# Kernel tuning notes

Hardware: AMD Instinct MI355X
Metric: run time of the kernel (lower is better)

## Reference

```python
import jax, jax.numpy as jnp
import numpy as np

B, H, W, D = 4, 256, 256, 128  # batch, height, width, channels (dim)
PAD = 1  # mask_padding -> band half-width


def setup_inputs() -> dict:
    key = jax.random.key(0)
    ks = jax.random.split(key, 6)
    s = 0.05  # weight init scale
    return {
        "x": jax.random.normal(ks[0], (B, H, W, D), jnp.float32),
        "kv": jax.random.normal(ks[1], (B, H, W, D), jnp.float32),
        "Wq_h": jax.random.normal(ks[2], (D, D), jnp.float32) * s,
        "Wk_h": jax.random.normal(ks[3], (D, D), jnp.float32) * s,
        "Wq_w": jax.random.normal(ks[4], (D, D), jnp.float32) * s,
        "Wk_w": jax.random.normal(ks[5], (D, D), jnp.float32) * s,
    }


def _band_mask(t, pad, dtype):
    # Equivalent to conv2d(identity, horizontal-line kernel): 1 where |i-j| <= pad
    i = jnp.arange(t)
    return (jnp.abs(i[:, None] - i[None, :]) <= pad).astype(dtype)


def _attend(xa, kva, Wq, Wk, pad):
    # xa, kva: [N, t, d]; heads==1 so dim_heads == d (per source early-return quirk)
    q = xa @ Wq.T                                   # [N, t, d]
    k = kva @ Wk.T                                  # [N, t, d]
    e = q.shape[-1]
    dots = jnp.einsum('bie,bje->bij', q, k) * (e ** -0.5)  # [N, t, t]
    mask = _band_mask(dots.shape[-1], pad, dots.dtype)
    dots = dots + (1.0 - mask) * (-30000.0)
    attn = jax.nn.softmax(dots, axis=-1)
    # NOTE: original multiplies attention weights with raw kv (not v projection)
    return jnp.einsum('bij,bjd->bid', attn, kva)    # [N, t, d]


def reference(x, kv, Wq_h, Wk_h, Wq_w, Wk_w):
    b, h, w, d = x.shape
    # Axis 1 (height): permutation [0,2,1,3]
    xh = jnp.transpose(x, (0, 2, 1, 3)).reshape(b * w, h, d)
    kvh = jnp.transpose(kv, (0, 2, 1, 3)).reshape(b * w, h, d)
    oh = _attend(xh, kvh, Wq_h, Wk_h, PAD).reshape(b, w, h, d)
    oh = jnp.transpose(oh, (0, 2, 1, 3))
    # Axis 2 (width): identity permutation [0,1,2,3]
    xw = x.reshape(b * h, w, d)
    kvw = kv.reshape(b * h, w, d)
    ow = _attend(xw, kvw, Wq_w, Wk_w, PAD).reshape(b, h, w, d)
    return oh + ow  # sum_axial_out=True
```

## Files before the change

kernel.cpp:

```cpp
#include <hip/hip_runtime.h>

#define DD    128
#define LINE  256
#define NPOS  262144
#define TILE  64
#define NROW  66
#define NROWP 80
#define LSTR  136

typedef __bf16 bf16x8 __attribute__((ext_vector_type(8)));
typedef float  f32x4v __attribute__((ext_vector_type(4)));
typedef float  f32x2v __attribute__((ext_vector_type(2)));
typedef unsigned int u32x2v __attribute__((ext_vector_type(2)));
typedef unsigned int u32x4v __attribute__((ext_vector_type(4)));

static __device__ __forceinline__ unsigned short f2bf(float f) {
  union { float f; unsigned u; } v; v.f = f;
  unsigned u = v.u + 0x7FFFu + ((v.u >> 16) & 1u);
  return (unsigned short)(u >> 16);
}
#define BF_LO(u) __uint_as_float((u) << 16)
#define BF_HI(u) __uint_as_float((u) & 0xffff0000u)


__global__ void make_mt_kernel(const float* __restrict__ Wq_h, const float* __restrict__ Wk_h,
                               const float* __restrict__ Wq_w, const float* __restrict__ Wk_w,
                               unsigned short* __restrict__ Ms) {
  const float* Wq = blockIdx.y ? Wq_w : Wq_h;
  const float* Wk = blockIdx.y ? Wk_w : Wk_h;
  unsigned short* M = Ms + blockIdx.y * (DD * DD);
  int d = blockIdx.x, c = threadIdx.x;
  float acc = 0.f;
  for (int e = 0; e < DD; ++e) acc += Wq[e * DD + c] * Wk[e * DD + d];
  M[d * DD + c] = f2bf(acc * 0.08838834764831845f);
}

__global__ __launch_bounds__(256) void project_kernel(const float* __restrict__ x,
                                                      const unsigned short* __restrict__ Mt,
                                                      unsigned short* __restrict__ XMh,
                                                      unsigned short* __restrict__ XMw) {
  __shared__ unsigned short x_s[64 * LSTR];
  const int tid = threadIdx.x;
  const long row0 = (long)blockIdx.x * 64;

  for (int u = tid; u < 64 * 32; u += 256) {
    int row = u >> 5, c4 = u & 31;
    f32x4v v = *(const f32x4v*)(x + (row0 + row) * DD + c4 * 4);
    u32x2v wv;
    wv.x = (unsigned)f2bf(v.x) | ((unsigned)f2bf(v.y) << 16);
    wv.y = (unsigned)f2bf(v.z) | ((unsigned)f2bf(v.w) << 16);
    *(u32x2v*)&x_s[row * LSTR + c4 * 4] = wv;
  }
  __syncthreads();

  const int wave = tid >> 6, lane = tid & 63;
  const int r16 = lane & 15, q = lane >> 4;
  const unsigned short* Mm = Mt + (wave >> 1) * (DD * DD);
  unsigned short* XO = (wave >> 1) ? XMw : XMh;

#pragma unroll
  for (int ci = 0; ci < 4; ++ci) {
    int ct = (wave & 1) * 4 + ci;
    bf16x8 b[4];
#pragma unroll
    for (int ks = 0; ks < 4; ++ks)
      b[ks] = __builtin_bit_cast(
          bf16x8, *(const u32x4v*)(Mm + (ct * 16 + r16) * DD + ks * 32 + q * 8));
#pragma unroll
    for (int rt = 0; rt < 4; ++rt) {
      f32x4v acc = {0.f, 0.f, 0.f, 0.f};
#pragma unroll
      for (int ks = 0; ks < 4; ++ks) {
        bf16x8 a = __builtin_bit_cast(
            bf16x8, *(const u32x4v*)&x_s[(rt * 16 + r16) * LSTR + ks * 32 + q * 8]);
        acc = __builtin_amdgcn_mfma_f32_16x16x32_bf16(a, b[ks], acc, 0, 0, 0);
      }
#pragma unroll
      for (int r = 0; r < 4; ++r) {
        long row = row0 + rt * 16 + q * 4 + r;
        XO[row * DD + ct * 16 + r16] = f2bf(acc[r]);
      }
    }
  }
}

static __device__ __forceinline__ float dot8(const float q[8], f32x4v a, f32x4v b) {
  return q[0] * a.x + q[1] * a.y + q[2] * a.z + q[3] * a.w
       + q[4] * b.x + q[5] * b.y + q[6] * b.z + q[7] * b.w;
}
static __device__ __forceinline__ float red16(float v) {
#pragma unroll
  for (int m = 1; m < 16; m <<= 1) v += __shfl_xor(v, m, 16);
  return v;
}
static __device__ __forceinline__ void dec4(unsigned lo, unsigned hi, float* q) {
  q[0] = BF_LO(lo); q[1] = BF_HI(lo); q[2] = BF_LO(hi); q[3] = BF_HI(hi);
}

__global__ __launch_bounds__(256) void band_kernel(const float* __restrict__ kv,
                                                   const unsigned short* __restrict__ XMh,
                                                   const unsigned short* __restrict__ XMw,
                                                   float* __restrict__ out) {
  const int tid = threadIdx.x;
  const int g = tid >> 4, l = tid & 15;
  const int w = blockIdx.x * 16 + g;
  const int y = blockIdx.y;
  const int h = y & 255;
  const long pos = (long)y * 256 + w;
  const long pn = (h > 0)    ? pos - 256 : pos;
  const long ps = (h < 255)  ? pos + 256 : pos;
  const long pw = (w > 0)    ? pos - 1   : pos;
  const long pe = (w < 255)  ? pos + 1   : pos;
  const int c0 = l * 4, c1 = 64 + l * 4;

  f32x4v cA = *(const f32x4v*)(kv + pos * DD + c0);
  f32x4v cB = *(const f32x4v*)(kv + pos * DD + c1);
  f32x4v nA = *(const f32x4v*)(kv + pn * DD + c0);
  f32x4v nB = *(const f32x4v*)(kv + pn * DD + c1);
  f32x4v sA = *(const f32x4v*)(kv + ps * DD + c0);
  f32x4v sB = *(const f32x4v*)(kv + ps * DD + c1);
  f32x4v wA = *(const f32x4v*)(kv + pw * DD + c0);
  f32x4v wB = *(const f32x4v*)(kv + pw * DD + c1);
  f32x4v eA = *(const f32x4v*)(kv + pe * DD + c0);
  f32x4v eB = *(const f32x4v*)(kv + pe * DD + c1);

  u32x2v xh0 = *(const u32x2v*)(XMh + pos * DD + c0);
  u32x2v xh1 = *(const u32x2v*)(XMh + pos * DD + c1);
  u32x2v xw0 = *(const u32x2v*)(XMw + pos * DD + c0);
  u32x2v xw1 = *(const u32x2v*)(XMw + pos * DD + c1);
  float qh[8], qw[8];
  dec4(xh0.x, xh0.y, qh); dec4(xh1.x, xh1.y, qh + 4);
  dec4(xw0.x, xw0.y, qw); dec4(xw1.x, xw1.y, qw + 4);

  float sh_n = red16(dot8(qh, nA, nB));
  float sh_c = red16(dot8(qh, cA, cB));
  float sh_s = red16(dot8(qh, sA, sB));
  float sw_w = red16(dot8(qw, wA, wB));
  float sw_c = red16(dot8(qw, cA, cB));
  float sw_e = red16(dot8(qw, eA, eB));

  if (h == 0)   sh_n = -1e30f;
  if (h == 255) sh_s = -1e30f;
  if (w == 0)   sw_w = -1e30f;
  if (w == 255) sw_e = -1e30f;

  float mh = fmaxf(sh_n, fmaxf(sh_c, sh_s));
  float e0 = __expf(sh_n - mh), e1 = __expf(sh_c - mh), e2 = __expf(sh_s - mh);
  float ih = 1.f / (e0 + e1 + e2);
  float ph0 = e0 * ih, ph1 = e1 * ih, ph2 = e2 * ih;

  float mw = fmaxf(sw_w, fmaxf(sw_c, sw_e));
  float f0 = __expf(sw_w - mw), f1 = __expf(sw_c - mw), f2 = __expf(sw_e - mw);
  float iw = 1.f / (f0 + f1 + f2);
  float pw0 = f0 * iw, pw1 = f1 * iw, pw2 = f2 * iw;

  float pc = ph1 + pw1;
  f32x4v oA, oB;
  oA.x = ph0 * nA.x + pc * cA.x + ph2 * sA.x + pw0 * wA.x + pw2 * eA.x;
  oA.y = ph0 * nA.y + pc * cA.y + ph2 * sA.y + pw0 * wA.y + pw2 * eA.y;
  oA.z = ph0 * nA.z + pc * cA.z + ph2 * sA.z + pw0 * wA.z + pw2 * eA.z;
  oA.w = ph0 * nA.w + pc * cA.w + ph2 * sA.w + pw0 * wA.w + pw2 * eA.w;
  oB.x = ph0 * nB.x + pc * cB.x + ph2 * sB.x + pw0 * wB.x + pw2 * eB.x;
  oB.y = ph0 * nB.y + pc * cB.y + ph2 * sB.y + pw0 * wB.y + pw2 * eB.y;
  oB.z = ph0 * nB.z + pc * cB.z + ph2 * sB.z + pw0 * wB.z + pw2 * eB.z;
  oB.w = ph0 * nB.w + pc * cB.w + ph2 * sB.w + pw0 * wB.w + pw2 * eB.w;
  *(f32x4v*)(out + pos * DD + c0) = oA;
  *(f32x4v*)(out + pos * DD + c1) = oB;
}

__global__ void make_m_kernel(const float* __restrict__ Wq_h, const float* __restrict__ Wk_h,
                              const float* __restrict__ Wq_w, const float* __restrict__ Wk_w,
                              unsigned short* __restrict__ Ms) {
  const float* Wq = blockIdx.y ? Wq_w : Wq_h;
  const float* Wk = blockIdx.y ? Wk_w : Wk_h;
  unsigned short* M = Ms + blockIdx.y * (DD * DD);
  int d = blockIdx.x, c = threadIdx.x;
  float acc = 0.f;
  for (int e = 0; e < DD; ++e) acc += Wq[e * DD + d] * Wk[e * DD + c];
  M[d * DD + c] = f2bf(acc * 0.08838834764831845f);
}

template <int AXIS, bool ADD>
__global__ __launch_bounds__(256) void axial_pass(const float* __restrict__ x,
                                                  const float* __restrict__ kv,
                                                  const unsigned short* __restrict__ M,
                                                  float* __restrict__ out) {
  __shared__ unsigned short kv_s[NROWP * LSTR];
  __shared__ unsigned short x_s[TILE * LSTR];
  __shared__ unsigned short kvm_s[NROW * LSTR];
  __shared__ float s_s[3 * TILE];
  __shared__ float p_s[3 * TILE];

  const int tid  = threadIdx.x;
  const int seg0 = blockIdx.x * TILE;
  const int line = blockIdx.y;

  size_t base; int stride;
  if (AXIS == 0) {
    int b = line >> 8, w = line & 255;
    base = (size_t)b * (256 * 256 * 128) + (size_t)w * DD;
    stride = 256 * 128;
  } else {
    base = (size_t)line * (256 * 128);
    stride = DD;
  }

  for (int u = tid; u < NROWP * 32; u += 256) {
    int row = u >> 5, c4 = u & 31;
    u32x2v wv; wv.x = 0u; wv.y = 0u;
    if (row < NROW) {
      int pos = seg0 - 1 + row;
      pos = pos < 0 ? 0 : (pos > LINE - 1 ? LINE - 1 : pos);
      f32x4v v = *(const f32x4v*)(kv + base + (size_t)pos * stride + c4 * 4);
      wv.x = (unsigned)f2bf(v.x) | ((unsigned)f2bf(v.y) << 16);
      wv.y = (unsigned)f2bf(v.z) | ((unsigned)f2bf(v.w) << 16);
    }
    *(u32x2v*)&kv_s[row * LSTR + c4 * 4] = wv;
  }
  for (int u = tid; u < TILE * 32; u += 256) {
    int row = u >> 5, c4 = u & 31;
    f32x4v v = *(const f32x4v*)(x + base + (size_t)(seg0 + row) * stride + c4 * 4);
    u32x2v wv;
    wv.x = (unsigned)f2bf(v.x) | ((unsigned)f2bf(v.y) << 16);
    wv.y = (unsigned)f2bf(v.z) | ((unsigned)f2bf(v.w) << 16);
    *(u32x2v*)&x_s[row * LSTR + c4 * 4] = wv;
  }
  __syncthreads();

  {
    const int wave = tid >> 6, lane = tid & 63;
    const int r16 = lane & 15, q = lane >> 4;
    for (int ct = wave * 2; ct < wave * 2 + 2; ++ct) {
      bf16x8 b[4];
#pragma unroll
      for (int ks = 0; ks < 4; ++ks)
        b[ks] = __builtin_bit_cast(
            bf16x8, *(const u32x4v*)(M + (ct * 16 + r16) * DD + ks * 32 + q * 8));
#pragma unroll
      for (int rt = 0; rt < 5; ++rt) {
        f32x4v acc = {0.f, 0.f, 0.f, 0.f};
#pragma unroll
        for (int ks = 0; ks < 4; ++ks) {
          bf16x8 a = __builtin_bit_cast(
              bf16x8, *(const u32x4v*)&kv_s[(rt * 16 + r16) * LSTR + ks * 32 + q * 8]);
          acc = __builtin_amdgcn_mfma_f32_16x16x32_bf16(a, b[ks], acc, 0, 0, 0);
        }
        int col = ct * 16 + r16;
#pragma unroll
        for (int r = 0; r < 4; ++r) {
          int row = rt * 16 + q * 4 + r;
          if (row < NROW) kvm_s[row * LSTR + col] = f2bf(acc[r]);
        }
      }
    }
  }
  __syncthreads();

  {
    int i = tid >> 2, sub = tid & 3;
    float s0 = 0.f, s1 = 0.f, s2 = 0.f;
#pragma unroll
    for (int ch = 0; ch < 4; ++ch) {
      int off = sub * 32 + ch * 8;
      float xf[8];
      {
        u32x4v t = *(const u32x4v*)&x_s[i * LSTR + off];
        xf[0] = BF_LO(t.x); xf[1] = BF_HI(t.x); xf[2] = BF_LO(t.y); xf[3] = BF_HI(t.y);
        xf[4] = BF_LO(t.z); xf[5] = BF_HI(t.z); xf[6] = BF_LO(t.w); xf[7] = BF_HI(t.w);
      }
      {
        u32x4v t = *(const u32x4v*)&kvm_s[(i + 0) * LSTR + off];
        s0 += xf[0]*BF_LO(t.x) + xf[1]*BF_HI(t.x) + xf[2]*BF_LO(t.y) + xf[3]*BF_HI(t.y)
            + xf[4]*BF_LO(t.z) + xf[5]*BF_HI(t.z) + xf[6]*BF_LO(t.w) + xf[7]*BF_HI(t.w);
      }
      {
        u32x4v t = *(const u32x4v*)&kvm_s[(i + 1) * LSTR + off];
        s1 += xf[0]*BF_LO(t.x) + xf[1]*BF_HI(t.x) + xf[2]*BF_LO(t.y) + xf[3]*BF_HI(t.y)
            + xf[4]*BF_LO(t.z) + xf[5]*BF_HI(t.z) + xf[6]*BF_LO(t.w) + xf[7]*BF_HI(t.w);
      }
      {
        u32x4v t = *(const u32x4v*)&kvm_s[(i + 2) * LSTR + off];
        s2 += xf[0]*BF_LO(t.x) + xf[1]*BF_HI(t.x) + xf[2]*BF_LO(t.y) + xf[3]*BF_HI(t.y)
            + xf[4]*BF_LO(t.z) + xf[5]*BF_HI(t.z) + xf[6]*BF_LO(t.w) + xf[7]*BF_HI(t.w);
      }
    }
    s0 += __shfl_xor(s0, 1); s0 += __shfl_xor(s0, 2);
    s1 += __shfl_xor(s1, 1); s1 += __shfl_xor(s1, 2);
    s2 += __shfl_xor(s2, 1); s2 += __shfl_xor(s2, 2);
    if (sub == 0) {
      int gp = seg0 + i;
      s_s[0 * TILE + i] = (gp - 1 >= 0)   ? s0 : -1e30f;
      s_s[1 * TILE + i] = s1;
      s_s[2 * TILE + i] = (gp + 1 < LINE) ? s2 : -1e30f;
    }
  }
  __syncthreads();

  if (tid < TILE) {
    float s0 = s_s[0 * TILE + tid], s1 = s_s[1 * TILE + tid], s2 = s_s[2 * TILE + tid];
    float m = fmaxf(s0, fmaxf(s1, s2));
    float e0 = __expf(s0 - m), e1 = __expf(s1 - m), e2 = __expf(s2 - m);
    float inv = 1.f / (e0 + e1 + e2);
    p_s[0 * TILE + tid] = e0 * inv;
    p_s[1 * TILE + tid] = e1 * inv;
    p_s[2 * TILE + tid] = e2 * inv;
  }
  __syncthreads();

  for (int r = 0; r < 16; ++r) {
    int u  = r * 256 + tid;
    int i  = u >> 6, dp = u & 63;
    float p0 = p_s[0 * TILE + i], p1 = p_s[1 * TILE + i], p2 = p_s[2 * TILE + i];
    unsigned a0 = *(const unsigned*)&kv_s[(i + 0) * LSTR + dp * 2];
    unsigned a1 = *(const unsigned*)&kv_s[(i + 1) * LSTR + dp * 2];
    unsigned a2 = *(const unsigned*)&kv_s[(i + 2) * LSTR + dp * 2];
    f32x2v o;
    o.x = p0 * BF_LO(a0) + p1 * BF_LO(a1) + p2 * BF_LO(a2);
    o.y = p0 * BF_HI(a0) + p1 * BF_HI(a1) + p2 * BF_HI(a2);
    size_t oidx = base + (size_t)(seg0 + i) * stride + dp * 2;
    if (ADD) {
      f32x2v prev = *(const f32x2v*)(out + oidx);
      o.x += prev.x; o.y += prev.y;
    }
    *(f32x2v*)(out + oidx) = o;
  }
}

extern "C" void kernel_launch(void* const* d_in, const int* in_sizes, int n_in,
                              void* d_out, int out_size, void* d_ws, size_t ws_size,
                              hipStream_t stream) {
  const float* x    = (const float*)d_in[0];
  const float* kv   = (const float*)d_in[1];
  const float* Wq_h = (const float*)d_in[2];
  const float* Wk_h = (const float*)d_in[3];
  const float* Wq_w = (const float*)d_in[4];
  const float* Wk_w = (const float*)d_in[5];
  float* out = (float*)d_out;

  const size_t ms_bytes = 2ull * DD * DD * 2;
  const size_t xm_bytes = (size_t)NPOS * DD * 2;
  const size_t need = ms_bytes + 2 * xm_bytes;

  if (ws_size >= need) {
    unsigned short* Ms  = (unsigned short*)d_ws;
    unsigned short* XMh = (unsigned short*)((char*)d_ws + ms_bytes);
    unsigned short* XMw = XMh + (size_t)NPOS * DD;

    make_mt_kernel<<<dim3(DD, 2), dim3(DD), 0, stream>>>(Wq_h, Wk_h, Wq_w, Wk_w, Ms);
    project_kernel<<<dim3(NPOS / 64), dim3(256), 0, stream>>>(x, Ms, XMh, XMw);
    band_kernel<<<dim3(LINE / 16, 4 * LINE), dim3(256), 0, stream>>>(kv, XMh, XMw, out);
  } else {
    unsigned short* Ms = (unsigned short*)d_ws;
    make_m_kernel<<<dim3(DD, 2), dim3(DD), 0, stream>>>(Wq_h, Wk_h, Wq_w, Wk_w, Ms);
    dim3 grid(LINE / TILE, 4 * 256);
    axial_pass<0, false><<<grid, dim3(256), 0, stream>>>(x, kv, Ms, out);
    axial_pass<1, true ><<<grid, dim3(256), 0, stream>>>(x, kv, Ms + DD * DD, out);
  }
}
```

Before: 436.9 us.

## Fuse projection and band attention into one kernel keeping projections in LDS

```diff
diff --git a/kernel.cpp b/kernel.cpp
--- a/kernel.cpp
+++ b/kernel.cpp
@@ -3,6 +3,7 @@
 #define DD    128
 #define LINE  256
 #define NPOS  262144
+#define BP    32
 #define TILE  64
 #define NROW  66
 #define NROWP 80
@@ -35,15 +36,33 @@
   M[d * DD + c] = f2bf(acc * 0.08838834764831845f);
 }
 
-__global__ __launch_bounds__(256) void project_kernel(const float* __restrict__ x,
-                                                      const unsigned short* __restrict__ Mt,
-                                                      unsigned short* __restrict__ XMh,
-                                                      unsigned short* __restrict__ XMw) {
-  __shared__ unsigned short x_s[64 * LSTR];
+static __device__ __forceinline__ float dot8(const float q[8], f32x4v a, f32x4v b) {
+  return q[0] * a.x + q[1] * a.y + q[2] * a.z + q[3] * a.w
+       + q[4] * b.x + q[5] * b.y + q[6] * b.z + q[7] * b.w;
+}
+static __device__ __forceinline__ float red16(float v) {
+#pragma unroll
+  for (int m = 1; m < 16; m <<= 1) v += __shfl_xor(v, m, 16);
+  return v;
+}
+static __device__ __forceinline__ void dec4(unsigned lo, unsigned hi, float* q) {
+  q[0] = BF_LO(lo); q[1] = BF_HI(lo); q[2] = BF_LO(hi); q[3] = BF_HI(hi);
+}
+
+__global__ __launch_bounds__(256) void fused_kernel(const float* __restrict__ x,
+                                                    const float* __restrict__ kv,
+                                                    const unsigned short* __restrict__ Mt,
+                                                    float* __restrict__ out) {
+  __shared__ unsigned short x_s[BP * LSTR];
+  __shared__ unsigned short xm_s[2 * BP * LSTR];
+
   const int tid = threadIdx.x;
-  const long row0 = (long)blockIdx.x * 64;
-
-  for (int u = tid; u < 64 * 32; u += 256) {
+  const int y  = blockIdx.y;
+  const int h  = y & 255;
+  const int w0 = blockIdx.x * BP;
+  const long row0 = (long)y * 256 + w0;
+
+  for (int u = tid; u < BP * 32; u += 256) {
     int row = u >> 5, c4 = u & 31;
     f32x4v v = *(const f32x4v*)(x + (row0 + row) * DD + c4 * 4);
     u32x2v wv;
@@ -53,119 +72,102 @@
   }
   __syncthreads();
 
-  const int wave = tid >> 6, lane = tid & 63;
-  const int r16 = lane & 15, q = lane >> 4;
-  const unsigned short* Mm = Mt + (wave >> 1) * (DD * DD);
-  unsigned short* XO = (wave >> 1) ? XMw : XMh;
-
-#pragma unroll
-  for (int ci = 0; ci < 4; ++ci) {
-    int ct = (wave & 1) * 4 + ci;
-    bf16x8 b[4];
-#pragma unroll
-    for (int ks = 0; ks < 4; ++ks)
-      b[ks] = __builtin_bit_cast(
-          bf16x8, *(const u32x4v*)(Mm + (ct * 16 + r16) * DD + ks * 32 + q * 8));
-#pragma unroll
-    for (int rt = 0; rt < 4; ++rt) {
-      f32x4v acc = {0.f, 0.f, 0.f, 0.f};
-#pragma unroll
-      for (int ks = 0; ks < 4; ++ks) {
-        bf16x8 a = __builtin_bit_cast(
-            bf16x8, *(const u32x4v*)&x_s[(rt * 16 + r16) * LSTR + ks * 32 + q * 8]);
-        acc = __builtin_amdgcn_mfma_f32_16x16x32_bf16(a, b[ks], acc, 0, 0, 0);
-      }
-#pragma unroll
-      for (int r = 0; r < 4; ++r) {
-        long row = row0 + rt * 16 + q * 4 + r;
-        XO[row * DD + ct * 16 + r16] = f2bf(acc[r]);
-      }
-    }
-  }
-}
-
-static __device__ __forceinline__ float dot8(const float q[8], f32x4v a, f32x4v b) {
-  return q[0] * a.x + q[1] * a.y + q[2] * a.z + q[3] * a.w
-       + q[4] * b.x + q[5] * b.y + q[6] * b.z + q[7] * b.w;
-}
-static __device__ __forceinline__ float red16(float v) {
-#pragma unroll
-  for (int m = 1; m < 16; m <<= 1) v += __shfl_xor(v, m, 16);
-  return v;
-}
-static __device__ __forceinline__ void dec4(unsigned lo, unsigned hi, float* q) {
-  q[0] = BF_LO(lo); q[1] = BF_HI(lo); q[2] = BF_LO(hi); q[3] = BF_HI(hi);
-}
-
-__global__ __launch_bounds__(256) void band_kernel(const float* __restrict__ kv,
-                                                   const unsigned short* __restrict__ XMh,
-                                                   const unsigned short* __restrict__ XMw,
-                                                   float* __restrict__ out) {
-  const int tid = threadIdx.x;
-  const int g = tid >> 4, l = tid & 15;
-  const int w = blockIdx.x * 16 + g;
-  const int y = blockIdx.y;
-  const int h = y & 255;
-  const long pos = (long)y * 256 + w;
-  const long pn = (h > 0)    ? pos - 256 : pos;
-  const long ps = (h < 255)  ? pos + 256 : pos;
-  const long pw = (w > 0)    ? pos - 1   : pos;
-  const long pe = (w < 255)  ? pos + 1   : pos;
-  const int c0 = l * 4, c1 = 64 + l * 4;
-
-  f32x4v cA = *(const f32x4v*)(kv + pos * DD + c0);
-  f32x4v cB = *(const f32x4v*)(kv + pos * DD + c1);
-  f32x4v nA = *(const f32x4v*)(kv + pn * DD + c0);
-  f32x4v nB = *(const f32x4v*)(kv + pn * DD + c1);
-  f32x4v sA = *(const f32x4v*)(kv + ps * DD + c0);
-  f32x4v sB = *(const f32x4v*)(kv + ps * DD + c1);
-  f32x4v wA = *(const f32x4v*)(kv + pw * DD + c0);
-  f32x4v wB = *(const f32x4v*)(kv + pw * DD + c1);
-  f32x4v eA = *(const f32x4v*)(kv + pe * DD + c0);
-  f32x4v eB = *(const f32x4v*)(kv + pe * DD + c1);
-
-  u32x2v xh0 = *(const u32x2v*)(XMh + pos * DD + c0);
-  u32x2v xh1 = *(const u32x2v*)(XMh + pos * DD + c1);
-  u32x2v xw0 = *(const u32x2v*)(XMw + pos * DD + c0);
-  u32x2v xw1 = *(const u32x2v*)(XMw + pos * DD + c1);
-  float qh[8], qw[8];
-  dec4(xh0.x, xh0.y, qh); dec4(xh1.x, xh1.y, qh + 4);
-  dec4(xw0.x, xw0.y, qw); dec4(xw1.x, xw1.y, qw + 4);
-
-  float sh_n = red16(dot8(qh, nA, nB));
-  float sh_c = red16(dot8(qh, cA, cB));
-  float sh_s = red16(dot8(qh, sA, sB));
-  float sw_w = red16(dot8(qw, wA, wB));
-  float sw_c = red16(dot8(qw, cA, cB));
-  float sw_e = red16(dot8(qw, eA, eB));
-
-  if (h == 0)   sh_n = -1e30f;
-  if (h == 255) sh_s = -1e30f;
-  if (w == 0)   sw_w = -1e30f;
-  if (w == 255) sw_e = -1e30f;
-
-  float mh = fmaxf(sh_n, fmaxf(sh_c, sh_s));
-  float e0 = __expf(sh_n - mh), e1 = __expf(sh_c - mh), e2 = __expf(sh_s - mh);
-  float ih = 1.f / (e0 + e1 + e2);
-  float ph0 = e0 * ih, ph1 = e1 * ih, ph2 = e2 * ih;
-
-  float mw = fmaxf(sw_w, fmaxf(sw_c, sw_e));
-  float f0 = __expf(sw_w - mw), f1 = __expf(sw_c - mw), f2 = __expf(sw_e - mw);
-  float iw = 1.f / (f0 + f1 + f2);
-  float pw0 = f0 * iw, pw1 = f1 * iw, pw2 = f2 * iw;
-
-  float pc = ph1 + pw1;
-  f32x4v oA, oB;
-  oA.x = ph0 * nA.x + pc * cA.x + ph2 * sA.x + pw0 * wA.x + pw2 * eA.x;
-  oA.y = ph0 * nA.y + pc * cA.y + ph2 * sA.y + pw0 * wA.y + pw2 * eA.y;
-  oA.z = ph0 * nA.z + pc * cA.z + ph2 * sA.z + pw0 * wA.z + pw2 * eA.z;
-  oA.w = ph0 * nA.w + pc * cA.w + ph2 * sA.w + pw0 * wA.w + pw2 * eA.w;
-  oB.x = ph0 * nB.x + pc * cB.x + ph2 * sB.x + pw0 * wB.x + pw2 * eB.x;
-  oB.y = ph0 * nB.y + pc * cB.y + ph2 * sB.y + pw0 * wB.y + pw2 * eB.y;
-  oB.z = ph0 * nB.z + pc * cB.z + ph2 * sB.z + pw0 * wB.z + pw2 * eB.z;
-  oB.w = ph0 * nB.w + pc * cB.w + ph2 * sB.w + pw0 * wB.w + pw2 * eB.w;
-  *(f32x4v*)(out + pos * DD + c0) = oA;
-  *(f32x4v*)(out + pos * DD + c1) = oB;
+  {
+    const int wave = tid >> 6, lane = tid & 63;
+    const int r16 = lane & 15, q = lane >> 4;
+    const unsigned short* Mm = Mt + (wave >> 1) * (DD * DD);
+    unsigned short* XO = xm_s + (wave >> 1) * (BP * LSTR);
+#pragma unroll
+    for (int ci = 0; ci < 4; ++ci) {
+      int ct = (wave & 1) * 4 + ci;
+      bf16x8 b[4];
+#pragma unroll
+      for (int ks = 0; ks < 4; ++ks)
+        b[ks] = __builtin_bit_cast(
+            bf16x8, *(const u32x4v*)(Mm + (ct * 16 + r16) * DD + ks * 32 + q * 8));
+#pragma unroll
+      for (int rt = 0; rt < BP / 16; ++rt) {
+        f32x4v acc = {0.f, 0.f, 0.f, 0.f};
+#pragma unroll
+        for (int ks = 0; ks < 4; ++ks) {
+          bf16x8 a = __builtin_bit_cast(
+              bf16x8, *(const u32x4v*)&x_s[(rt * 16 + r16) * LSTR + ks * 32 + q * 8]);
+          acc = __builtin_amdgcn_mfma_f32_16x16x32_bf16(a, b[ks], acc, 0, 0, 0);
+        }
+#pragma unroll
+        for (int r = 0; r < 4; ++r) {
+          int row = rt * 16 + q * 4 + r;
+          XO[row * LSTR + ct * 16 + r16] = f2bf(acc[r]);
+        }
+      }
+    }
+  }
+  __syncthreads();
+
+  for (int it = 0; it < BP / 16; ++it) {
+    const int g = it * 16 + (tid >> 4), l = tid & 15;
+    const int w = w0 + g;
+    const long pos = row0 + g;
+    const long pn = (h > 0)   ? pos - 256 : pos;
+    const long ps = (h < 255) ? pos + 256 : pos;
+    const long pw = (w > 0)   ? pos - 1   : pos;
+    const long pe = (w < 255) ? pos + 1   : pos;
+    const int c0 = l * 4, c1 = 64 + l * 4;
+
+    f32x4v cA = *(const f32x4v*)(kv + pos * DD + c0);
+    f32x4v cB = *(const f32x4v*)(kv + pos * DD + c1);
+    f32x4v nA = *(const f32x4v*)(kv + pn * DD + c0);
+    f32x4v nB = *(const f32x4v*)(kv + pn * DD + c1);
+    f32x4v sA = *(const f32x4v*)(kv + ps * DD + c0);
+    f32x4v sB = *(const f32x4v*)(kv + ps * DD + c1);
+    f32x4v wA = *(const f32x4v*)(kv + pw * DD + c0);
+    f32x4v wB = *(const f32x4v*)(kv + pw * DD + c1);
+    f32x4v eA = *(const f32x4v*)(kv + pe * DD + c0);
+    f32x4v eB = *(const f32x4v*)(kv + pe * DD + c1);
+
+    u32x2v xh0 = *(const u32x2v*)&xm_s[g * LSTR + c0];
+    u32x2v xh1 = *(const u32x2v*)&xm_s[g * LSTR + c1];
+    u32x2v xw0 = *(const u32x2v*)&xm_s[BP * LSTR + g * LSTR + c0];
+    u32x2v xw1 = *(const u32x2v*)&xm_s[BP * LSTR + g * LSTR + c1];
+    float qh[8], qw[8];
+    dec4(xh0.x, xh0.y, qh); dec4(xh1.x, xh1.y, qh + 4);
+    dec4(xw0.x, xw0.y, qw); dec4(xw1.x, xw1.y, qw + 4);
+
+    float sh_n = red16(dot8(qh, nA, nB));
+    float sh_c = red16(dot8(qh, cA, cB));
+    float sh_s = red16(dot8(qh, sA, sB));
+    float sw_w = red16(dot8(qw, wA, wB));
+    float sw_c = red16(dot8(qw, cA, cB));
+    float sw_e = red16(dot8(qw, eA, eB));
+
+    if (h == 0)   sh_n = -1e30f;
+    if (h == 255) sh_s = -1e30f;
+    if (w == 0)   sw_w = -1e30f;
+    if (w == 255) sw_e = -1e30f;
+
+    float mh = fmaxf(sh_n, fmaxf(sh_c, sh_s));
+    float e0 = __expf(sh_n - mh), e1 = __expf(sh_c - mh), e2 = __expf(sh_s - mh);
+    float ih = 1.f / (e0 + e1 + e2);
+    float ph0 = e0 * ih, ph1 = e1 * ih, ph2 = e2 * ih;
+
+    float mw = fmaxf(sw_w, fmaxf(sw_c, sw_e));
+    float f0 = __expf(sw_w - mw), f1 = __expf(sw_c - mw), f2 = __expf(sw_e - mw);
+    float iw = 1.f / (f0 + f1 + f2);
+    float pw0 = f0 * iw, pw1 = f1 * iw, pw2 = f2 * iw;
+
+    float pc = ph1 + pw1;
+    f32x4v oA, oB;
+    oA.x = ph0 * nA.x + pc * cA.x + ph2 * sA.x + pw0 * wA.x + pw2 * eA.x;
+    oA.y = ph0 * nA.y + pc * cA.y + ph2 * sA.y + pw0 * wA.y + pw2 * eA.y;
+    oA.z = ph0 * nA.z + pc * cA.z + ph2 * sA.z + pw0 * wA.z + pw2 * eA.z;
+    oA.w = ph0 * nA.w + pc * cA.w + ph2 * sA.w + pw0 * wA.w + pw2 * eA.w;
+    oB.x = ph0 * nB.x + pc * cB.x + ph2 * sB.x + pw0 * wB.x + pw2 * eB.x;
+    oB.y = ph0 * nB.y + pc * cB.y + ph2 * sB.y + pw0 * wB.y + pw2 * eB.y;
+    oB.z = ph0 * nB.z + pc * cB.z + ph2 * sB.z + pw0 * wB.z + pw2 * eB.z;
+    oB.w = ph0 * nB.w + pc * cB.w + ph2 * sB.w + pw0 * wB.w + pw2 * eB.w;
+    *(f32x4v*)(out + pos * DD + c0) = oA;
+    *(f32x4v*)(out + pos * DD + c1) = oB;
+  }
 }
 
 __global__ void make_m_kernel(const float* __restrict__ Wq_h, const float* __restrict__ Wk_h,
@@ -338,17 +340,11 @@
   float* out = (float*)d_out;
 
   const size_t ms_bytes = 2ull * DD * DD * 2;
-  const size_t xm_bytes = (size_t)NPOS * DD * 2;
-  const size_t need = ms_bytes + 2 * xm_bytes;
-
-  if (ws_size >= need) {
-    unsigned short* Ms  = (unsigned short*)d_ws;
-    unsigned short* XMh = (unsigned short*)((char*)d_ws + ms_bytes);
-    unsigned short* XMw = XMh + (size_t)NPOS * DD;
-
+
+  if (ws_size >= ms_bytes) {
+    unsigned short* Ms = (unsigned short*)d_ws;
     make_mt_kernel<<<dim3(DD, 2), dim3(DD), 0, stream>>>(Wq_h, Wk_h, Wq_w, Wk_w, Ms);
-    project_kernel<<<dim3(NPOS / 64), dim3(256), 0, stream>>>(x, Ms, XMh, XMw);
-    band_kernel<<<dim3(LINE / 16, 4 * LINE), dim3(256), 0, stream>>>(kv, XMh, XMw, out);
+    fused_kernel<<<dim3(LINE / BP, 4 * LINE), dim3(256), 0, stream>>>(x, kv, Ms, out);
   } else {
     unsigned short* Ms = (unsigned short*)d_ws;
     make_m_kernel<<<dim3(DD, 2), dim3(DD), 0, stream>>>(Wq_h, Wk_h, Wq_w, Wk_w, Ms);
```

Result: faster. 359.5 us (-17.7%).
